# Performance work log

Hardware: AMD Instinct MI355X
Metric: run time of the kernel (lower is better)

## Reference

```python
import jax, jax.numpy as jnp
import numpy as np

B, L, V, E, H = 16, 256, 32000, 256, 256


def setup_inputs() -> dict:
    key = jax.random.key(0)
    k_ids, k_len, k_emb, k1, k2, k3, k4, k5, k6, k7, k8 = jax.random.split(key, 11)
    # lengths: sorted descending, max length == L (pack_padded_sequence convention)
    lengths = jnp.sort(jax.random.randint(k_len, (B,), 1, L + 1))[::-1]
    lengths = lengths.at[0].set(L).astype(jnp.int32)
    # token ids; positions >= length use padding index 0
    ids = jax.random.randint(k_ids, (B, L), 1, V)
    tmask = jnp.arange(L)[None, :] < lengths[:, None]
    ids = jnp.where(tmask, ids, 0)
    seq = jax.nn.one_hot(ids, V, dtype=jnp.float32)  # [B, L, V] one-hot
    # embedding table, padding_idx=0 row zeroed
    emb_weight = jax.random.normal(k_emb, (V, E), jnp.float32) * 0.05
    emb_weight = emb_weight.at[0].set(0.0)
    s = 0.05
    W_ih_f = jax.random.normal(k1, (4 * H, E), jnp.float32) * s
    W_hh_f = jax.random.normal(k2, (4 * H, H), jnp.float32) * s
    b_f = jax.random.normal(k3, (4 * H,), jnp.float32) * s
    W_ih_b = jax.random.normal(k4, (4 * H, E), jnp.float32) * s
    W_hh_b = jax.random.normal(k5, (4 * H, H), jnp.float32) * s
    b_b = jax.random.normal(k6, (4 * H,), jnp.float32) * s
    return {"seq": seq, "emb_weight": emb_weight,
            "W_ih_f": W_ih_f, "W_hh_f": W_hh_f, "b_f": b_f,
            "W_ih_b": W_ih_b, "W_hh_b": W_hh_b, "b_b": b_b,
            "lengths": lengths}


def _lstm_scan(x_seq, mask_seq, W_ih, W_hh, b):
    # x_seq: [L, B, E], mask_seq: [L, B] (True = valid timestep)
    h0 = jnp.zeros((x_seq.shape[1], W_hh.shape[1]), x_seq.dtype)
    c0 = jnp.zeros_like(h0)

    def step(carry, inp):
        h, c = carry
        x, m = inp
        gates = x @ W_ih.T + h @ W_hh.T + b
        i, f, g, o = jnp.split(gates, 4, axis=-1)  # torch gate order i,f,g,o
        i = jax.nn.sigmoid(i); f = jax.nn.sigmoid(f)
        g = jnp.tanh(g); o = jax.nn.sigmoid(o)
        c_new = f * c + i * g
        h_new = o * jnp.tanh(c_new)
        m = m[:, None]
        h2 = jnp.where(m, h_new, h)
        c2 = jnp.where(m, c_new, c)
        out = jnp.where(m, h_new, 0.0)  # pad_packed pads with 0
        return (h2, c2), out

    _, outs = jax.lax.scan(step, (h0, c0), (x_seq, mask_seq))
    return outs


def reference(seq, emb_weight, W_ih_f, W_hh_f, b_f, W_ih_b, W_hh_b, b_b, lengths):
    # one-hot matmul embedding (faithful to torch.matmul(seq, embedding.weight))
    embedding = jnp.einsum('blv,ve->ble', seq, emb_weight)  # [B, L, E]
    x = embedding.transpose(1, 0, 2)                        # [L, B, E]
    Lax = x.shape[0]
    mask = jnp.arange(Lax)[:, None] < lengths[None, :]      # [L, B]
    out_f = _lstm_scan(x, mask, W_ih_f, W_hh_f, b_f)
    out_b = _lstm_scan(x[::-1], mask[::-1], W_ih_b, W_hh_b, b_b)[::-1]
    output = jnp.concatenate([out_f, out_b], axis=-1).transpose(1, 0, 2)  # [B, L, 2H]
    return output
```

## Files before the change

kernel.cpp:

```cpp
#include <hip/hip_runtime.h>
#include <cstddef>
#include <cstdint>

#define HX_OFF   0
#define FLG_OFF  32768
#define MS_BYTES 33280
#define X_OFF    65536
#define G_OFF    (X_OFF + 4096 * 256 * 4)

typedef __attribute__((ext_vector_type(8))) short short8;
typedef __attribute__((ext_vector_type(4))) float f32x4;
typedef __attribute__((ext_vector_type(2))) unsigned long long ulong2v;

__device__ __forceinline__ unsigned short f2bf(float f) {
  unsigned u = __builtin_bit_cast(unsigned, f);
  u = (u + 0x7fffu + ((u >> 16) & 1u)) >> 16;
  return (unsigned short)u;
}

__global__ __launch_bounds__(256) void k_embed(const float* __restrict__ seq,
                                               const float* __restrict__ emb,
                                               float* __restrict__ x) {
  const int m = blockIdx.x;
  const int t = m >> 4, b = m & 15;
  const float* row = seq + (size_t)(b * 256 + t) * 32000;
  __shared__ int sid;
  if (threadIdx.x == 0) sid = 0;
  __syncthreads();
  for (int base = threadIdx.x * 4; base < 32000; base += 1024) {
    const float4 v = *reinterpret_cast<const float4*>(row + base);
    if (v.x != 0.f) sid = base;
    if (v.y != 0.f) sid = base + 1;
    if (v.z != 0.f) sid = base + 2;
    if (v.w != 0.f) sid = base + 3;
  }
  __syncthreads();
  x[(size_t)m * 256 + threadIdx.x] = emb[(size_t)sid * 256 + threadIdx.x];
}

__global__ __launch_bounds__(256) void k_gemm(const float* __restrict__ x,
                                              const float* __restrict__ Wf,
                                              const float* __restrict__ Wb,
                                              const float* __restrict__ bf,
                                              const float* __restrict__ bb,
                                              float* __restrict__ Gm) {
  __shared__ float As[8][128];
  __shared__ float Bs[8][128];
  const int tid = threadIdx.x;
  const int m0 = (blockIdx.x >> 4) * 128;
  const int n0 = (blockIdx.x & 15) * 128;
  const int lm = tid >> 1;
  const int lk = (tid & 1) * 4;
  const int nrow = n0 + lm;
  const float* wrow = (nrow < 1024) ? (Wf + (size_t)nrow * 256)
                                    : (Wb + (size_t)(nrow - 1024) * 256);
  const float* arow = x + (size_t)(m0 + lm) * 256;
  const int tm = (tid >> 4) * 8;
  const int tn = (tid & 15) * 8;
  float acc[8][8] = {};
  for (int k0 = 0; k0 < 256; k0 += 8) {
    const float4 av = *reinterpret_cast<const float4*>(arow + k0 + lk);
    const float4 wv = *reinterpret_cast<const float4*>(wrow + k0 + lk);
    __syncthreads();
    As[lk + 0][lm] = av.x; As[lk + 1][lm] = av.y; As[lk + 2][lm] = av.z; As[lk + 3][lm] = av.w;
    Bs[lk + 0][lm] = wv.x; Bs[lk + 1][lm] = wv.y; Bs[lk + 2][lm] = wv.z; Bs[lk + 3][lm] = wv.w;
    __syncthreads();
#pragma unroll
    for (int k = 0; k < 8; ++k) {
      float a[8], b[8];
      *reinterpret_cast<float4*>(&a[0]) = *reinterpret_cast<const float4*>(&As[k][tm]);
      *reinterpret_cast<float4*>(&a[4]) = *reinterpret_cast<const float4*>(&As[k][tm + 4]);
      *reinterpret_cast<float4*>(&b[0]) = *reinterpret_cast<const float4*>(&Bs[k][tn]);
      *reinterpret_cast<float4*>(&b[4]) = *reinterpret_cast<const float4*>(&Bs[k][tn + 4]);
#pragma unroll
      for (int i = 0; i < 8; ++i)
#pragma unroll
        for (int j = 0; j < 8; ++j) acc[i][j] = fmaf(a[i], b[j], acc[i][j]);
    }
  }
  float bj[8];
#pragma unroll
  for (int j = 0; j < 8; ++j) {
    const int nn = n0 + tn + j;
    bj[j] = (nn < 1024) ? bf[nn] : bb[nn - 1024];
  }
#pragma unroll
  for (int i = 0; i < 8; ++i) {
    float4 o0, o1;
    o0.x = acc[i][0] + bj[0]; o0.y = acc[i][1] + bj[1]; o0.z = acc[i][2] + bj[2]; o0.w = acc[i][3] + bj[3];
    o1.x = acc[i][4] + bj[4]; o1.y = acc[i][5] + bj[5]; o1.z = acc[i][6] + bj[6]; o1.w = acc[i][7] + bj[7];
    float* op = Gm + (size_t)(m0 + tm + i) * 2048 + n0 + tn;
    *reinterpret_cast<float4*>(op) = o0;
    *reinterpret_cast<float4*>(op + 4) = o1;
  }
}

__global__ __launch_bounds__(256, 1) void k_scan(const float* __restrict__ Whf,
                                                 const float* __restrict__ Whb,
                                                 const int* __restrict__ lengths,
                                                 const float* __restrict__ Gm,
                                                 unsigned short* hx,
                                                 unsigned int* flags,
                                                 float* __restrict__ out) {
  const int wg = blockIdx.x;
  const int d = wg >> 2;
  const int widx = wg & 3;
  const int j0 = widx * 64;
  const float* Wh = d ? Whb : Whf;
  const int tid = threadIdx.x;
  const int wv = tid >> 6;
  const int l = tid & 63;
  const int lr = l & 15;
  const int kg = l >> 4;
  const int jrel = wv * 16 + lr;
  const int j = j0 + jrel;

  short8 wfrag[4][8];
#pragma unroll
  for (int g = 0; g < 4; ++g) {
#pragma unroll
    for (int ks = 0; ks < 8; ++ks) {
      const float* wp = Wh + (size_t)(g * 256 + j) * 256 + ks * 32 + kg * 8;
      const float4 w0 = *reinterpret_cast<const float4*>(wp);
      const float4 w1 = *reinterpret_cast<const float4*>(wp + 4);
      short8 wv8;
      wv8[0] = (short)f2bf(w0.x); wv8[1] = (short)f2bf(w0.y);
      wv8[2] = (short)f2bf(w0.z); wv8[3] = (short)f2bf(w0.w);
      wv8[4] = (short)f2bf(w1.x); wv8[5] = (short)f2bf(w1.y);
      wv8[6] = (short)f2bf(w1.z); wv8[7] = (short)f2bf(w1.w);
      wfrag[g][ks] = wv8;
    }
  }

  int len4[4];
#pragma unroll
  for (int r = 0; r < 4; ++r) len4[r] = lengths[kg * 4 + r];

  float c_st[4] = {0.f, 0.f, 0.f, 0.f}, h_st[4] = {0.f, 0.f, 0.f, 0.f};

  __shared__ unsigned short h_stage[16][64];

  unsigned short* hxd = hx + d * 2 * 4096;
  unsigned int* myflag = flags + (d * 4 + widx) * 16;
  const unsigned int* spinflag = flags + (d * 4 + (l & 3)) * 16;

  for (int s = 0; s < 256; ++s) {
    const int t = d ? (255 - s) : s;
    f32x4 acc[4];
    {
      const float* gp = Gm + (size_t)(t * 16 + kg * 4) * 2048 + d * 1024 + j;
#pragma unroll
      for (int g = 0; g < 4; ++g) {
#pragma unroll
        for (int r = 0; r < 4; ++r)
          acc[g][r] = gp[(size_t)r * 2048 + g * 256];
      }
    }
    if (s > 0) {
      unsigned v = __hip_atomic_load(spinflag, __ATOMIC_RELAXED, __HIP_MEMORY_SCOPE_AGENT);
      while (!__all(v >= (unsigned)s)) {
        __builtin_amdgcn_s_sleep(1);
        v = __hip_atomic_load(spinflag, __ATOMIC_RELAXED, __HIP_MEMORY_SCOPE_AGENT);
      }
    }
    short8 afrag[8];
    {
      const unsigned long long* hq =
          reinterpret_cast<const unsigned long long*>(hxd + (s & 1) * 4096);
      const int base = lr * 64 + kg * 2;
#pragma unroll
      for (int ks = 0; ks < 8; ++ks) {
        const unsigned long long q0 = __hip_atomic_load(hq + base + ks * 8, __ATOMIC_RELAXED, __HIP_MEMORY_SCOPE_AGENT);
        const unsigned long long q1 = __hip_atomic_load(hq + base + ks * 8 + 1, __ATOMIC_RELAXED, __HIP_MEMORY_SCOPE_AGENT);
        ulong2v q; q.x = q0; q.y = q1;
        afrag[ks] = __builtin_bit_cast(short8, q);
      }
    }
#pragma unroll
    for (int ks = 0; ks < 8; ++ks) {
#pragma unroll
      for (int g = 0; g < 4; ++g)
        acc[g] = __builtin_amdgcn_mfma_f32_16x16x32_bf16(afrag[ks], wfrag[g][ks], acc[g], 0, 0, 0);
    }
    float hout[4];
#pragma unroll
    for (int r = 0; r < 4; ++r) {
      const float gi = acc[0][r], gf = acc[1][r], gg = acc[2][r], go = acc[3][r];
      const float ig = 1.f / (1.f + __expf(-gi));
      const float fg = 1.f / (1.f + __expf(-gf));
      const float gt = tanhf(gg);
      const float og = 1.f / (1.f + __expf(-go));
      const float cn = fmaf(fg, c_st[r], ig * gt);
      const float hn = og * tanhf(cn);
      const bool msk = t < len4[r];
      c_st[r] = msk ? cn : c_st[r];
      h_st[r] = msk ? hn : h_st[r];
      hout[r] = msk ? hn : 0.f;
    }
    if (s < 255) {
#pragma unroll
      for (int r = 0; r < 4; ++r) h_stage[kg * 4 + r][jrel] = f2bf(h_st[r]);
      __syncthreads();
      {
        const int b_ = tid >> 4, jq = (tid & 15) * 4;
        const unsigned long long v =
            *reinterpret_cast<const unsigned long long*>(&h_stage[b_][jq]);
        unsigned long long* dq =
            reinterpret_cast<unsigned long long*>(hxd + ((s + 1) & 1) * 4096);
        __hip_atomic_store(dq + b_ * 64 + (j0 + jq) / 4, v,
                           __ATOMIC_RELAXED, __HIP_MEMORY_SCOPE_AGENT);
      }
      asm volatile("s_waitcnt vmcnt(0)" ::: "memory");
      __syncthreads();
      if (tid == 0)
        __hip_atomic_store(myflag, (unsigned)(s + 1), __ATOMIC_RELAXED, __HIP_MEMORY_SCOPE_AGENT);
    }
    {
      float* op = out + ((size_t)(kg * 4) * 256 + t) * 512 + d * 256 + j;
#pragma unroll
      for (int r = 0; r < 4; ++r) op[(size_t)r * 256 * 512] = hout[r];
    }
  }
}

extern "C" void kernel_launch(void* const* d_in, const int* in_sizes, int n_in,
                              void* d_out, int out_size, void* d_ws, size_t ws_size,
                              hipStream_t stream) {
  const float* seq = (const float*)d_in[0];
  const float* emb = (const float*)d_in[1];
  const float* Wif = (const float*)d_in[2];
  const float* Whf = (const float*)d_in[3];
  const float* bf  = (const float*)d_in[4];
  const float* Wib = (const float*)d_in[5];
  const float* Whb = (const float*)d_in[6];
  const float* bbv = (const float*)d_in[7];
  const int* lengths = (const int*)d_in[8];
  float* out = (float*)d_out;
  char* ws = (char*)d_ws;
  float* x  = (float*)(ws + X_OFF);
  float* Gm = (float*)(ws + G_OFF);
  unsigned short* hx = (unsigned short*)(ws + HX_OFF);
  unsigned int* flags = (unsigned int*)(ws + FLG_OFF);

  hipMemsetAsync(d_ws, 0, MS_BYTES, stream);
  k_embed<<<dim3(4096), dim3(256), 0, stream>>>(seq, emb, x);
  k_gemm<<<dim3(512), dim3(256), 0, stream>>>(x, Wif, Wib, bf, bbv, Gm);
  k_scan<<<dim3(8), dim3(256), 0, stream>>>(Whf, Whb, lengths, Gm, hx, flags, out);
}
```

Before: 1.834 ms.

## Tag hidden-state words with step counters, use bf16 MFMA input GEMM

The scan kernel drops the per-workgroup flag barrier and LDS staging. Each lane now writes its hidden value as a 32-bit word holding a step tag and the bf16 value, and readers spin until every tag matches, so data and synchronisation travel together. The input projection GEMM moves from an fp32 SIMT kernel to bf16 MFMA, fed by a bf16 embedding buffer and a separate weight cast kernel, and the gate activations use fast reciprocal-based sigmoid and tanh. This doubles the hx buffer footprint and lowers precision of the input projection in exchange for shorter cross-workgroup latency per step.

```diff
diff --git a/kernel.cpp b/kernel.cpp
--- a/kernel.cpp
+++ b/kernel.cpp
@@ -3,24 +3,33 @@
 #include <cstdint>
 
 #define HX_OFF   0
-#define FLG_OFF  32768
-#define MS_BYTES 33280
+#define MS_BYTES 65536
 #define X_OFF    65536
-#define G_OFF    (X_OFF + 4096 * 256 * 4)
+#define W_OFF    (X_OFF + 4096 * 256 * 2)
+#define G_OFF    (W_OFF + 2048 * 256 * 2)
 
 typedef __attribute__((ext_vector_type(8))) short short8;
 typedef __attribute__((ext_vector_type(4))) float f32x4;
-typedef __attribute__((ext_vector_type(2))) unsigned long long ulong2v;
+typedef __attribute__((ext_vector_type(4))) unsigned uint4v;
 
 __device__ __forceinline__ unsigned short f2bf(float f) {
   unsigned u = __builtin_bit_cast(unsigned, f);
   u = (u + 0x7fffu + ((u >> 16) & 1u)) >> 16;
   return (unsigned short)u;
 }
+__device__ __forceinline__ float sigm_f(float x) {
+  return __builtin_amdgcn_rcpf(1.f + __expf(-x));
+}
+__device__ __forceinline__ float tanh_f(float x) {
+  return 1.f - 2.f * __builtin_amdgcn_rcpf(1.f + __expf(2.f * x));
+}
+__device__ __forceinline__ unsigned pack_lo16(unsigned long long q) {
+  return ((unsigned)q & 0xFFFFu) | ((unsigned)(q >> 32) << 16);
+}
 
 __global__ __launch_bounds__(256) void k_embed(const float* __restrict__ seq,
                                                const float* __restrict__ emb,
-                                               float* __restrict__ x) {
+                                               unsigned short* __restrict__ xb) {
   const int m = blockIdx.x;
   const int t = m >> 4, b = m & 15;
   const float* row = seq + (size_t)(b * 256 + t) * 32000;
@@ -35,63 +44,49 @@
     if (v.w != 0.f) sid = base + 3;
   }
   __syncthreads();
-  x[(size_t)m * 256 + threadIdx.x] = emb[(size_t)sid * 256 + threadIdx.x];
-}
-
-__global__ __launch_bounds__(256) void k_gemm(const float* __restrict__ x,
-                                              const float* __restrict__ Wf,
+  xb[(size_t)m * 256 + threadIdx.x] = f2bf(emb[(size_t)sid * 256 + threadIdx.x]);
+}
+
+__global__ __launch_bounds__(256) void k_cast(const float* __restrict__ Wf,
                                               const float* __restrict__ Wb,
+                                              unsigned short* __restrict__ Wc) {
+  const int e = (blockIdx.x * 256 + threadIdx.x) * 4;
+  const float* src = (e < 1024 * 256) ? (Wf + e) : (Wb + (e - 1024 * 256));
+  const float4 v = *reinterpret_cast<const float4*>(src);
+  ushort4 o;
+  o.x = f2bf(v.x); o.y = f2bf(v.y); o.z = f2bf(v.z); o.w = f2bf(v.w);
+  *reinterpret_cast<ushort4*>(Wc + e) = o;
+}
+
+__global__ __launch_bounds__(256) void k_gemm(const unsigned short* __restrict__ Xb,
+                                              const unsigned short* __restrict__ Wc,
                                               const float* __restrict__ bf,
                                               const float* __restrict__ bb,
                                               float* __restrict__ Gm) {
-  __shared__ float As[8][128];
-  __shared__ float Bs[8][128];
   const int tid = threadIdx.x;
-  const int m0 = (blockIdx.x >> 4) * 128;
-  const int n0 = (blockIdx.x & 15) * 128;
-  const int lm = tid >> 1;
-  const int lk = (tid & 1) * 4;
-  const int nrow = n0 + lm;
-  const float* wrow = (nrow < 1024) ? (Wf + (size_t)nrow * 256)
-                                    : (Wb + (size_t)(nrow - 1024) * 256);
-  const float* arow = x + (size_t)(m0 + lm) * 256;
-  const int tm = (tid >> 4) * 8;
-  const int tn = (tid & 15) * 8;
-  float acc[8][8] = {};
-  for (int k0 = 0; k0 < 256; k0 += 8) {
-    const float4 av = *reinterpret_cast<const float4*>(arow + k0 + lk);
-    const float4 wv = *reinterpret_cast<const float4*>(wrow + k0 + lk);
-    __syncthreads();
-    As[lk + 0][lm] = av.x; As[lk + 1][lm] = av.y; As[lk + 2][lm] = av.z; As[lk + 3][lm] = av.w;
-    Bs[lk + 0][lm] = wv.x; Bs[lk + 1][lm] = wv.y; Bs[lk + 2][lm] = wv.z; Bs[lk + 3][lm] = wv.w;
-    __syncthreads();
-#pragma unroll
-    for (int k = 0; k < 8; ++k) {
-      float a[8], b[8];
-      *reinterpret_cast<float4*>(&a[0]) = *reinterpret_cast<const float4*>(&As[k][tm]);
-      *reinterpret_cast<float4*>(&a[4]) = *reinterpret_cast<const float4*>(&As[k][tm + 4]);
-      *reinterpret_cast<float4*>(&b[0]) = *reinterpret_cast<const float4*>(&Bs[k][tn]);
-      *reinterpret_cast<float4*>(&b[4]) = *reinterpret_cast<const float4*>(&Bs[k][tn + 4]);
-#pragma unroll
-      for (int i = 0; i < 8; ++i)
-#pragma unroll
-        for (int j = 0; j < 8; ++j) acc[i][j] = fmaf(a[i], b[j], acc[i][j]);
-    }
-  }
-  float bj[8];
-#pragma unroll
-  for (int j = 0; j < 8; ++j) {
-    const int nn = n0 + tn + j;
-    bj[j] = (nn < 1024) ? bf[nn] : bb[nn - 1024];
-  }
-#pragma unroll
-  for (int i = 0; i < 8; ++i) {
-    float4 o0, o1;
-    o0.x = acc[i][0] + bj[0]; o0.y = acc[i][1] + bj[1]; o0.z = acc[i][2] + bj[2]; o0.w = acc[i][3] + bj[3];
-    o1.x = acc[i][4] + bj[4]; o1.y = acc[i][5] + bj[5]; o1.z = acc[i][6] + bj[6]; o1.w = acc[i][7] + bj[7];
-    float* op = Gm + (size_t)(m0 + tm + i) * 2048 + n0 + tn;
-    *reinterpret_cast<float4*>(op) = o0;
-    *reinterpret_cast<float4*>(op + 4) = o1;
+  const int wv = tid >> 6, l = tid & 63, lr = l & 15, kg = l >> 4;
+  const int m0 = (blockIdx.x >> 5) * 64;
+  const int n0 = (blockIdx.x & 31) * 64;
+  const int mrow = m0 + wv * 16 + lr;
+  short8 afrag[8];
+#pragma unroll
+  for (int ks = 0; ks < 8; ++ks)
+    afrag[ks] = *reinterpret_cast<const short8*>(Xb + (size_t)mrow * 256 + ks * 32 + kg * 8);
+#pragma unroll
+  for (int nt = 0; nt < 4; ++nt) {
+    const int n = n0 + nt * 16 + lr;
+    short8 bfrag[8];
+#pragma unroll
+    for (int ks = 0; ks < 8; ++ks)
+      bfrag[ks] = *reinterpret_cast<const short8*>(Wc + (size_t)n * 256 + ks * 32 + kg * 8);
+    f32x4 acc = {0.f, 0.f, 0.f, 0.f};
+#pragma unroll
+    for (int ks = 0; ks < 8; ++ks)
+      acc = __builtin_amdgcn_mfma_f32_16x16x32_bf16(afrag[ks], bfrag[ks], acc, 0, 0, 0);
+    const float bias = (n < 1024) ? bf[n] : bb[n - 1024];
+#pragma unroll
+    for (int r = 0; r < 4; ++r)
+      Gm[(size_t)(m0 + wv * 16 + kg * 4 + r) * 2048 + n] = acc[r] + bias;
   }
 }
 
@@ -99,8 +94,7 @@
                                                  const float* __restrict__ Whb,
                                                  const int* __restrict__ lengths,
                                                  const float* __restrict__ Gm,
-                                                 unsigned short* hx,
-                                                 unsigned int* flags,
+                                                 unsigned* hx,
                                                  float* __restrict__ out) {
   const int wg = blockIdx.x;
   const int d = wg >> 2;
@@ -112,8 +106,7 @@
   const int l = tid & 63;
   const int lr = l & 15;
   const int kg = l >> 4;
-  const int jrel = wv * 16 + lr;
-  const int j = j0 + jrel;
+  const int j = j0 + wv * 16 + lr;
 
   short8 wfrag[4][8];
 #pragma unroll
@@ -138,11 +131,7 @@
 
   float c_st[4] = {0.f, 0.f, 0.f, 0.f}, h_st[4] = {0.f, 0.f, 0.f, 0.f};
 
-  __shared__ unsigned short h_stage[16][64];
-
-  unsigned short* hxd = hx + d * 2 * 4096;
-  unsigned int* myflag = flags + (d * 4 + widx) * 16;
-  const unsigned int* spinflag = flags + (d * 4 + (l & 3)) * 16;
+  unsigned* hxd = hx + d * 2 * 4096;
 
   for (int s = 0; s < 256; ++s) {
     const int t = d ? (255 - s) : s;
@@ -156,25 +145,33 @@
           acc[g][r] = gp[(size_t)r * 2048 + g * 256];
       }
     }
-    if (s > 0) {
-      unsigned v = __hip_atomic_load(spinflag, __ATOMIC_RELAXED, __HIP_MEMORY_SCOPE_AGENT);
-      while (!__all(v >= (unsigned)s)) {
-        __builtin_amdgcn_s_sleep(1);
-        v = __hip_atomic_load(spinflag, __ATOMIC_RELAXED, __HIP_MEMORY_SCOPE_AGENT);
-      }
-    }
     short8 afrag[8];
     {
       const unsigned long long* hq =
           reinterpret_cast<const unsigned long long*>(hxd + (s & 1) * 4096);
-      const int base = lr * 64 + kg * 2;
-#pragma unroll
-      for (int ks = 0; ks < 8; ++ks) {
-        const unsigned long long q0 = __hip_atomic_load(hq + base + ks * 8, __ATOMIC_RELAXED, __HIP_MEMORY_SCOPE_AGENT);
-        const unsigned long long q1 = __hip_atomic_load(hq + base + ks * 8 + 1, __ATOMIC_RELAXED, __HIP_MEMORY_SCOPE_AGENT);
-        ulong2v q; q.x = q0; q.y = q1;
-        afrag[ks] = __builtin_bit_cast(short8, q);
-      }
+      const unsigned long long expv =
+          ((unsigned long long)s << 16) | ((unsigned long long)s << 48);
+      const int base0 = lr * 128 + kg * 4;
+      unsigned long long bad;
+      do {
+        bad = 0;
+#pragma unroll
+        for (int ks = 0; ks < 8; ++ks) {
+          const unsigned long long* p = hq + base0 + ks * 16;
+          const unsigned long long q0 = __hip_atomic_load(p + 0, __ATOMIC_RELAXED, __HIP_MEMORY_SCOPE_AGENT);
+          const unsigned long long q1 = __hip_atomic_load(p + 1, __ATOMIC_RELAXED, __HIP_MEMORY_SCOPE_AGENT);
+          const unsigned long long q2 = __hip_atomic_load(p + 2, __ATOMIC_RELAXED, __HIP_MEMORY_SCOPE_AGENT);
+          const unsigned long long q3 = __hip_atomic_load(p + 3, __ATOMIC_RELAXED, __HIP_MEMORY_SCOPE_AGENT);
+          bad |= (q0 ^ expv) & 0xFFFF0000FFFF0000ULL;
+          bad |= (q1 ^ expv) & 0xFFFF0000FFFF0000ULL;
+          bad |= (q2 ^ expv) & 0xFFFF0000FFFF0000ULL;
+          bad |= (q3 ^ expv) & 0xFFFF0000FFFF0000ULL;
+          uint4v u;
+          u.x = pack_lo16(q0); u.y = pack_lo16(q1);
+          u.z = pack_lo16(q2); u.w = pack_lo16(q3);
+          afrag[ks] = __builtin_bit_cast(short8, u);
+        }
+      } while (__any(bad != 0ULL));
     }
 #pragma unroll
     for (int ks = 0; ks < 8; ++ks) {
@@ -185,41 +182,28 @@
     float hout[4];
 #pragma unroll
     for (int r = 0; r < 4; ++r) {
-      const float gi = acc[0][r], gf = acc[1][r], gg = acc[2][r], go = acc[3][r];
-      const float ig = 1.f / (1.f + __expf(-gi));
-      const float fg = 1.f / (1.f + __expf(-gf));
-      const float gt = tanhf(gg);
-      const float og = 1.f / (1.f + __expf(-go));
+      const float ig = sigm_f(acc[0][r]);
+      const float fg = sigm_f(acc[1][r]);
+      const float gt = tanh_f(acc[2][r]);
+      const float og = sigm_f(acc[3][r]);
       const float cn = fmaf(fg, c_st[r], ig * gt);
-      const float hn = og * tanhf(cn);
+      const float hn = og * tanh_f(cn);
       const bool msk = t < len4[r];
       c_st[r] = msk ? cn : c_st[r];
       h_st[r] = msk ? hn : h_st[r];
       hout[r] = msk ? hn : 0.f;
     }
     if (s < 255) {
-#pragma unroll
-      for (int r = 0; r < 4; ++r) h_stage[kg * 4 + r][jrel] = f2bf(h_st[r]);
-      __syncthreads();
-      {
-        const int b_ = tid >> 4, jq = (tid & 15) * 4;
-        const unsigned long long v =
-            *reinterpret_cast<const unsigned long long*>(&h_stage[b_][jq]);
-        unsigned long long* dq =
-            reinterpret_cast<unsigned long long*>(hxd + ((s + 1) & 1) * 4096);
-        __hip_atomic_store(dq + b_ * 64 + (j0 + jq) / 4, v,
+      unsigned* dst = hxd + ((s + 1) & 1) * 4096;
+      const unsigned tagv = (unsigned)(s + 1) << 16;
+#pragma unroll
+      for (int r = 0; r < 4; ++r)
+        __hip_atomic_store(dst + (kg * 4 + r) * 256 + j, tagv | (unsigned)f2bf(h_st[r]),
                            __ATOMIC_RELAXED, __HIP_MEMORY_SCOPE_AGENT);
-      }
-      asm volatile("s_waitcnt vmcnt(0)" ::: "memory");
-      __syncthreads();
-      if (tid == 0)
-        __hip_atomic_store(myflag, (unsigned)(s + 1), __ATOMIC_RELAXED, __HIP_MEMORY_SCOPE_AGENT);
-    }
-    {
-      float* op = out + ((size_t)(kg * 4) * 256 + t) * 512 + d * 256 + j;
-#pragma unroll
-      for (int r = 0; r < 4; ++r) op[(size_t)r * 256 * 512] = hout[r];
-    }
+    }
+#pragma unroll
+    for (int r = 0; r < 4; ++r)
+      out[((size_t)(kg * 4 + r) * 256 + t) * 512 + d * 256 + j] = hout[r];
   }
 }
 
@@ -237,13 +221,14 @@
   const int* lengths = (const int*)d_in[8];
   float* out = (float*)d_out;
   char* ws = (char*)d_ws;
-  float* x  = (float*)(ws + X_OFF);
+  unsigned short* xb = (unsigned short*)(ws + X_OFF);
+  unsigned short* wc = (unsigned short*)(ws + W_OFF);
   float* Gm = (float*)(ws + G_OFF);
-  unsigned short* hx = (unsigned short*)(ws + HX_OFF);
-  unsigned int* flags = (unsigned int*)(ws + FLG_OFF);
+  unsigned* hx = (unsigned*)(ws + HX_OFF);
 
   hipMemsetAsync(d_ws, 0, MS_BYTES, stream);
-  k_embed<<<dim3(4096), dim3(256), 0, stream>>>(seq, emb, x);
-  k_gemm<<<dim3(512), dim3(256), 0, stream>>>(x, Wif, Wib, bf, bbv, Gm);
-  k_scan<<<dim3(8), dim3(256), 0, stream>>>(Whf, Whb, lengths, Gm, hx, flags, out);
-}
+  k_embed<<<dim3(4096), dim3(256), 0, stream>>>(seq, emb, xb);
+  k_cast<<<dim3(512), dim3(256), 0, stream>>>(Wif, Wib, wc);
+  k_gemm<<<dim3(2048), dim3(256), 0, stream>>>(xb, wc, bf, bbv, Gm);
+  k_scan<<<dim3(8), dim3(256), 0, stream>>>(Whf, Whb, lengths, Gm, hx, out);
+}
```

Measured after the change: 3.088 ms. 68.4% more time.
